# Performance work log

Measured on AMD Instinct MI355X. Metric: run time of the kernel, lower is better.

## Reference

```python
import jax, jax.numpy as jnp
import numpy as np

EMBED_DIM = 768
HEAD_SIZE = 64

def setup_inputs() -> dict:
    key = jax.random.key(0)
    k1, k2, k3, k4 = jax.random.split(key, 4)
    x = jax.random.normal(k1, (4, 4096, EMBED_DIM), dtype=jnp.float32)
    # nn.Linear(E, H, bias=False) weights, stored as [E, H] for y = x @ W
    scale = 1.0 / np.sqrt(EMBED_DIM)
    Wk = jax.random.uniform(k2, (EMBED_DIM, HEAD_SIZE), jnp.float32, -scale, scale)
    Wq = jax.random.uniform(k3, (EMBED_DIM, HEAD_SIZE), jnp.float32, -scale, scale)
    Wv = jax.random.uniform(k4, (EMBED_DIM, HEAD_SIZE), jnp.float32, -scale, scale)
    return {"x": x, "Wk": Wk, "Wq": Wq, "Wv": Wv}

def reference(x, Wk, Wq, Wv):
    # x: [B, S, E]
    E = x.shape[2]
    K = jnp.einsum("bse,eh->bsh", x, Wk)  # [B, S, H]
    Q = jnp.einsum("bse,eh->bsh", x, Wq)
    V = jnp.einsum("bse,eh->bsh", x, Wv)
    # NOTE: original scales by embedding_dim**0.5, not head_size**0.5
    A = jnp.einsum("bqh,bkh->bqk", Q, K) / jnp.sqrt(jnp.asarray(E, x.dtype))
    A = jax.nn.softmax(A, axis=-1)
    # dropout is inference-mode identity
    return jnp.einsum("bqk,bkh->bqh", A, V)
```

## Files before the change

### kernel.cpp

```cpp
#include <hip/hip_runtime.h>

typedef __attribute__((ext_vector_type(8))) short short8;
typedef __attribute__((ext_vector_type(4))) short short4v;
typedef __attribute__((ext_vector_type(4))) float float4v;

__device__ __forceinline__ short f2bf(float f) {
    union { float f; unsigned u; } v; v.f = f;
    return (short)((v.u + 0x7fffu + ((v.u >> 16) & 1u)) >> 16);
}

__device__ __forceinline__ float fast_exp2(float x) {
#if __has_builtin(__builtin_amdgcn_exp2f)
    return __builtin_amdgcn_exp2f(x);
#else
    return exp2f(x);
#endif
}

__global__ void wtrans_kernel(const float* __restrict__ Wk, const float* __restrict__ Wq,
                              const float* __restrict__ Wv, short* __restrict__ Wt3T) {
    int idx = blockIdx.x * 256 + threadIdx.x;
    int p = idx / 12288;
    int rem = idx - p * 12288;
    int kstep = rem / 512;
    int r2 = rem - kstep * 512;
    int lane = r2 >> 3, i = r2 & 7;
    int quad = lane >> 4, l16 = lane & 15;
    int j = p >> 2, nt = p & 3;
    int n = nt * 16 + l16;
    int k = kstep * 32 + quad * 8 + i;
    const float* W = (j == 0) ? Wq : (j == 1 ? Wk : Wv);
    float scale = (j == 0) ? 0.05205877f : 1.0f;
    Wt3T[idx] = f2bf(W[k * 64 + n] * scale);
}

__global__ __launch_bounds__(256, 4) void proj_kernel(
    const float* __restrict__ x, const short* __restrict__ Wt3T,
    short* __restrict__ Qs, short* __restrict__ Kb, short* __restrict__ Vtr)
{
    __shared__ alignas(16) int Abuf[3][256];
    __shared__ alignas(16) short sm[16 * 72];
    const int tid = threadIdx.x;
    const int wave = tid >> 6, lane = tid & 63, quad = lane >> 4, l16 = lane & 15;
    const int m0 = blockIdx.x * 16;
    const int p0 = wave * 3;

    const int xrow = tid >> 4, xcol = (tid & 15) * 2;
    const float* xp = x + (size_t)(m0 + xrow) * 768 + xcol;
    const int aidx = xrow * 16 + (tid & 15);
    const short* wt0 = Wt3T + (size_t)(p0 * 24) * 512 + lane * 8;

    float4v acc[3];
#pragma unroll
    for (int t = 0; t < 3; ++t) acc[t] = (float4v){0.f, 0.f, 0.f, 0.f};

    {
        float2 u = *(const float2*)xp;
        Abuf[0][aidx] = ((unsigned short)f2bf(u.x)) | ((unsigned)f2bf(u.y) << 16);
    }
    short8 Wc0 = *(const short8*)(wt0);
    short8 Wc1 = *(const short8*)(wt0 + 12288);
    short8 Wc2 = *(const short8*)(wt0 + 24576);
    float2 Xn = *(const float2*)(xp + 32);
    __syncthreads();

#pragma unroll
    for (int it = 0; it < 24; ++it) {
        short8 Wn0, Wn1, Wn2;
        float2 Xn2;
        if (it < 23) {
            const short* wn = wt0 + (it + 1) * 512;
            Wn0 = *(const short8*)(wn);
            Wn1 = *(const short8*)(wn + 12288);
            Wn2 = *(const short8*)(wn + 24576);
        }
        if (it < 22) Xn2 = *(const float2*)(xp + (it + 2) * 32);

        short8 a = *(const short8*)((const short*)Abuf[it % 3] + l16 * 32 + quad * 8);
        acc[0] = __builtin_amdgcn_mfma_f32_16x16x32_bf16(a, Wc0, acc[0], 0, 0, 0);
        acc[1] = __builtin_amdgcn_mfma_f32_16x16x32_bf16(a, Wc1, acc[1], 0, 0, 0);
        acc[2] = __builtin_amdgcn_mfma_f32_16x16x32_bf16(a, Wc2, acc[2], 0, 0, 0);

        if (it < 23)
            Abuf[(it + 1) % 3][aidx] = ((unsigned short)f2bf(Xn.x)) | ((unsigned)f2bf(Xn.y) << 16);
        Xn = Xn2;
        Wc0 = Wn0; Wc1 = Wn1; Wc2 = Wn2;
        __syncthreads();
    }

#pragma unroll
    for (int t = 0; t < 3; ++t) {
        const int p = p0 + t, j = p >> 2, nt = p & 3;
        if (j < 2) {
            short* dst = (j == 0) ? Qs : Kb;
#pragma unroll
            for (int r = 0; r < 4; ++r)
                dst[(size_t)(m0 + quad * 4 + r) * 64 + nt * 16 + l16] = f2bf(acc[t][r]);
        } else {
#pragma unroll
            for (int r = 0; r < 4; ++r)
                sm[(quad * 4 + r) * 72 + nt * 16 + l16] = f2bf(acc[t][r]);
        }
    }
    __syncthreads();
    {
        const int h = tid >> 2, si = (tid & 3) * 4;
        const int b = m0 >> 12, s0 = m0 & 4095;
        short4v tmp;
#pragma unroll
        for (int i = 0; i < 4; ++i) tmp[i] = sm[(si + i) * 72 + h];
        *(short4v*)(Vtr + (size_t)(b * 64 + h) * 4096 + s0 + si) = tmp;
    }
}

__global__ __launch_bounds__(256, 4) void attn_kernel(
    const short* __restrict__ Qs, const short* __restrict__ Kb, const short* __restrict__ Vt,
    float* __restrict__ Opart, float* __restrict__ Ll, int kv_len)
{
    __shared__ alignas(16) short Kl[64 * 72];
    __shared__ alignas(16) short Vl[64 * 72];
    __shared__ alignas(16) short Pl[4 * 32 * 72];

    const int tid = threadIdx.x;
    const int wave = tid >> 6, lane = tid & 63, quad = lane >> 4, l16 = lane & 15;
    const int qt = blockIdx.x, b = blockIdx.y, sp = blockIdx.z;
    const int q0 = qt * 128;
    const int bS = b * 4096;
    const int kv0 = sp * kv_len;

    short8 qa[2][2];
#pragma unroll
    for (int mt = 0; mt < 2; ++mt)
#pragma unroll
        for (int ks = 0; ks < 2; ++ks)
            qa[mt][ks] = *(const short8*)(Qs + (size_t)(bS + q0 + wave * 32 + mt * 16 + l16) * 64 + ks * 32 + quad * 8);

    float4v o[2][4];
    float rs[2][4];
#pragma unroll
    for (int mt = 0; mt < 2; ++mt)
#pragma unroll
        for (int nt = 0; nt < 4; ++nt) o[mt][nt] = (float4v){0.f, 0.f, 0.f, 0.f};
#pragma unroll
    for (int mt = 0; mt < 2; ++mt)
#pragma unroll
        for (int r = 0; r < 4; ++r) rs[mt][r] = 0.f;

    const int sr = tid >> 2, sc = (tid & 3) * 16;
    short* plw = &Pl[wave * 2304];

    for (int kt = 0; kt < kv_len; kt += 64) {
        const int kvg = kv0 + kt;
        __syncthreads();
        {
            const short* src = Kb + (size_t)(bS + kvg + sr) * 64 + sc;
            *(short8*)&Kl[sr * 72 + sc]     = *(const short8*)src;
            *(short8*)&Kl[sr * 72 + sc + 8] = *(const short8*)(src + 8);
            const short* vs = Vt + (size_t)(b * 64 + sr) * 4096 + kvg + sc;
            *(short8*)&Vl[sr * 72 + sc]     = *(const short8*)vs;
            *(short8*)&Vl[sr * 72 + sc + 8] = *(const short8*)(vs + 8);
        }
        __syncthreads();

        float4v s[2][4];
#pragma unroll
        for (int nt = 0; nt < 4; ++nt) {
            short8 b0 = *(const short8*)&Kl[(nt * 16 + l16) * 72 + quad * 8];
            short8 b1 = *(const short8*)&Kl[(nt * 16 + l16) * 72 + 32 + quad * 8];
#pragma unroll
            for (int mt = 0; mt < 2; ++mt) {
                float4v a0 = (float4v){0.f, 0.f, 0.f, 0.f};
                a0 = __builtin_amdgcn_mfma_f32_16x16x32_bf16(qa[mt][0], b0, a0, 0, 0, 0);
                a0 = __builtin_amdgcn_mfma_f32_16x16x32_bf16(qa[mt][1], b1, a0, 0, 0, 0);
                s[mt][nt] = a0;
            }
        }

#pragma unroll
        for (int mt = 0; mt < 2; ++mt)
#pragma unroll
            for (int nt = 0; nt < 4; ++nt)
#pragma unroll
                for (int r = 0; r < 4; ++r) {
                    float p = fast_exp2(s[mt][nt][r]);
                    rs[mt][r] += p;
                    plw[(mt * 16 + quad * 4 + r) * 72 + nt * 16 + l16] = f2bf(p);
                }

#pragma unroll
        for (int ks = 0; ks < 2; ++ks) {
            short8 bf[4];
#pragma unroll
            for (int nt = 0; nt < 4; ++nt)
                bf[nt] = *(const short8*)&Vl[(nt * 16 + l16) * 72 + ks * 32 + quad * 8];
#pragma unroll
            for (int mt = 0; mt < 2; ++mt) {
                short8 af = *(const short8*)&plw[(mt * 16 + l16) * 72 + ks * 32 + quad * 8];
#pragma unroll
                for (int nt = 0; nt < 4; ++nt)
                    o[mt][nt] = __builtin_amdgcn_mfma_f32_16x16x32_bf16(af, bf[nt], o[mt][nt], 0, 0, 0);
            }
        }
    }

#pragma unroll
    for (int mt = 0; mt < 2; ++mt)
#pragma unroll
        for (int r = 0; r < 4; ++r) {
#pragma unroll
            for (int off = 8; off >= 1; off >>= 1)
                rs[mt][r] += __shfl_xor(rs[mt][r], off);
        }

#pragma unroll
    for (int mt = 0; mt < 2; ++mt) {
#pragma unroll
        for (int nt = 0; nt < 4; ++nt)
#pragma unroll
            for (int r = 0; r < 4; ++r) {
                int qb = q0 + wave * 32 + mt * 16 + quad * 4 + r;
                Opart[((size_t)sp * 16384 + bS + qb) * 64 + nt * 16 + l16] = o[mt][nt][r];
            }
        if (l16 == 0) {
#pragma unroll
            for (int r = 0; r < 4; ++r) {
                int qb = q0 + wave * 32 + mt * 16 + quad * 4 + r;
                Ll[(size_t)sp * 16384 + bS + qb] = rs[mt][r];
            }
        }
    }
}

__global__ void combine_kernel(const float* __restrict__ Opart, const float* __restrict__ Ll,
                               float* __restrict__ out, int nsplit) {
    int idx = blockIdx.x * 256 + threadIdx.x;
    int q = idx >> 6;
    float den = 0.f, num = 0.f;
    for (int s = 0; s < nsplit; ++s) {
        den += Ll[s * 16384 + q];
        num += Opart[(size_t)s * 1048576 + idx];
    }
    out[idx] = num / den;
}

extern "C" void kernel_launch(void* const* d_in, const int* in_sizes, int n_in,
                              void* d_out, int out_size, void* d_ws, size_t ws_size,
                              hipStream_t stream) {
    const float* x  = (const float*)d_in[0];
    const float* Wk = (const float*)d_in[1];
    const float* Wq = (const float*)d_in[2];
    const float* Wv = (const float*)d_in[3];
    float* out = (float*)d_out;

    char* w = (char*)d_ws;
    size_t off = 0;
    auto take = [&](size_t bytes) -> void* {
        void* p = w + off;
        off = (off + bytes + 255) & ~(size_t)255;
        return p;
    };
    short* Qs  = (short*)take((size_t)16384 * 64 * 2);
    short* Kb  = (short*)take((size_t)16384 * 64 * 2);
    short* Vt  = (short*)take((size_t)16384 * 64 * 2);
    short* Wt3 = (short*)take((size_t)3 * 64 * 768 * 2);

    size_t base = off;
    int nsplit = 8;
    while (nsplit > 1) {
        size_t need = base + (((size_t)nsplit * 16384 * 4 + 255) & ~(size_t)255)
                      + (size_t)nsplit * 16384 * 64 * 4 + 512;
        if (need <= ws_size) break;
        nsplit >>= 1;
    }
    float* Ll    = (float*)take((size_t)nsplit * 16384 * 4);
    float* Opart = (float*)take((size_t)nsplit * 16384 * 64 * 4);

    wtrans_kernel<<<576, 256, 0, stream>>>(Wk, Wq, Wv, Wt3);
    proj_kernel<<<1024, 256, 0, stream>>>(x, Wt3, Qs, Kb, Vt);
    dim3 ag(32, 4, nsplit);
    attn_kernel<<<ag, 256, 0, stream>>>(Qs, Kb, Vt, Opart, Ll, 4096 / nsplit);
    combine_kernel<<<4096, 256, 0, stream>>>(Opart, Ll, out, nsplit);
}
```

Baseline: 144.8 us.

## Prefetch next K/V tile into registers and transpose S MFMA for packed P stores

Loads the next K and V tile from global memory into registers while the current tile is computed, replacing the load-then-wait pattern before each LDS fill. Swaps the MFMA operands so S is computed transposed: each lane then holds four consecutive keys for one query, which allows packed bf16 conversion with v_cvt_pk_bf16_f32 and 8-byte stores of P. The same layout shortens the row-sum reduction to two cross-lane shuffles. It also raises wave priority around the MFMA blocks. The prefetch adds register pressure under launch bounds of 4 blocks per CU.

```diff
diff --git a/kernel.cpp b/kernel.cpp
--- a/kernel.cpp
+++ b/kernel.cpp
@@ -3,6 +3,7 @@
 typedef __attribute__((ext_vector_type(8))) short short8;
 typedef __attribute__((ext_vector_type(4))) short short4v;
 typedef __attribute__((ext_vector_type(4))) float float4v;
+typedef __attribute__((ext_vector_type(2))) unsigned int uint2v;
 
 __device__ __forceinline__ short f2bf(float f) {
     union { float f; unsigned u; } v; v.f = f;
@@ -15,6 +16,12 @@
 #else
     return exp2f(x);
 #endif
+}
+
+__device__ __forceinline__ unsigned cvt_pk_bf16(float lo, float hi) {
+    unsigned r;
+    asm("v_cvt_pk_bf16_f32 %0, %1, %2" : "=v"(r) : "v"(lo), "v"(hi));
+    return r;
 }
 
 __global__ void wtrans_kernel(const float* __restrict__ Wk, const float* __restrict__ Wq,
@@ -128,64 +135,74 @@
     const int bS = b * 4096;
     const int kv0 = sp * kv_len;
 
-    short8 qa[2][2];
-#pragma unroll
-    for (int mt = 0; mt < 2; ++mt)
+    short8 qb[2][2];
+#pragma unroll
+    for (int ntq = 0; ntq < 2; ++ntq)
 #pragma unroll
         for (int ks = 0; ks < 2; ++ks)
-            qa[mt][ks] = *(const short8*)(Qs + (size_t)(bS + q0 + wave * 32 + mt * 16 + l16) * 64 + ks * 32 + quad * 8);
+            qb[ntq][ks] = *(const short8*)(Qs + (size_t)(bS + q0 + wave * 32 + ntq * 16 + l16) * 64 + ks * 32 + quad * 8);
 
     float4v o[2][4];
-    float rs[2][4];
-#pragma unroll
-    for (int mt = 0; mt < 2; ++mt)
-#pragma unroll
-        for (int nt = 0; nt < 4; ++nt) o[mt][nt] = (float4v){0.f, 0.f, 0.f, 0.f};
-#pragma unroll
-    for (int mt = 0; mt < 2; ++mt)
-#pragma unroll
-        for (int r = 0; r < 4; ++r) rs[mt][r] = 0.f;
+#pragma unroll
+    for (int ntq = 0; ntq < 2; ++ntq)
+#pragma unroll
+        for (int nt = 0; nt < 4; ++nt) o[ntq][nt] = (float4v){0.f, 0.f, 0.f, 0.f};
+    float rs[2] = {0.f, 0.f};
 
     const int sr = tid >> 2, sc = (tid & 3) * 16;
     short* plw = &Pl[wave * 2304];
 
-    for (int kt = 0; kt < kv_len; kt += 64) {
-        const int kvg = kv0 + kt;
+    const short* ksrc0 = Kb + (size_t)(bS + kv0 + sr) * 64 + sc;
+    const short* vsrc0 = Vt + (size_t)(b * 64 + sr) * 4096 + kv0 + sc;
+
+    short8 kr0 = *(const short8*)ksrc0;
+    short8 kr1 = *(const short8*)(ksrc0 + 8);
+    short8 vr0 = *(const short8*)vsrc0;
+    short8 vr1 = *(const short8*)(vsrc0 + 8);
+
+    const int ntiles = kv_len >> 6;
+    for (int t = 0; t < ntiles; ++t) {
         __syncthreads();
-        {
-            const short* src = Kb + (size_t)(bS + kvg + sr) * 64 + sc;
-            *(short8*)&Kl[sr * 72 + sc]     = *(const short8*)src;
-            *(short8*)&Kl[sr * 72 + sc + 8] = *(const short8*)(src + 8);
-            const short* vs = Vt + (size_t)(b * 64 + sr) * 4096 + kvg + sc;
-            *(short8*)&Vl[sr * 72 + sc]     = *(const short8*)vs;
-            *(short8*)&Vl[sr * 72 + sc + 8] = *(const short8*)(vs + 8);
-        }
+        *(short8*)&Kl[sr * 72 + sc]     = kr0;
+        *(short8*)&Kl[sr * 72 + sc + 8] = kr1;
+        *(short8*)&Vl[sr * 72 + sc]     = vr0;
+        *(short8*)&Vl[sr * 72 + sc + 8] = vr1;
         __syncthreads();
 
-        float4v s[2][4];
-#pragma unroll
-        for (int nt = 0; nt < 4; ++nt) {
-            short8 b0 = *(const short8*)&Kl[(nt * 16 + l16) * 72 + quad * 8];
-            short8 b1 = *(const short8*)&Kl[(nt * 16 + l16) * 72 + 32 + quad * 8];
-#pragma unroll
-            for (int mt = 0; mt < 2; ++mt) {
-                float4v a0 = (float4v){0.f, 0.f, 0.f, 0.f};
-                a0 = __builtin_amdgcn_mfma_f32_16x16x32_bf16(qa[mt][0], b0, a0, 0, 0, 0);
-                a0 = __builtin_amdgcn_mfma_f32_16x16x32_bf16(qa[mt][1], b1, a0, 0, 0, 0);
-                s[mt][nt] = a0;
-            }
-        }
-
-#pragma unroll
-        for (int mt = 0; mt < 2; ++mt)
-#pragma unroll
-            for (int nt = 0; nt < 4; ++nt)
-#pragma unroll
-                for (int r = 0; r < 4; ++r) {
-                    float p = fast_exp2(s[mt][nt][r]);
-                    rs[mt][r] += p;
-                    plw[(mt * 16 + quad * 4 + r) * 72 + nt * 16 + l16] = f2bf(p);
-                }
+        if (t + 1 < ntiles) {
+            const short* kn = ksrc0 + (size_t)(t + 1) * 4096;
+            kr0 = *(const short8*)kn;
+            kr1 = *(const short8*)(kn + 8);
+            const short* vn = vsrc0 + (t + 1) * 64;
+            vr0 = *(const short8*)vn;
+            vr1 = *(const short8*)(vn + 8);
+        }
+
+#pragma unroll
+        for (int mtk = 0; mtk < 4; ++mtk) {
+            short8 k0 = *(const short8*)&Kl[(mtk * 16 + l16) * 72 + quad * 8];
+            short8 k1 = *(const short8*)&Kl[(mtk * 16 + l16) * 72 + 32 + quad * 8];
+            float4v s0 = (float4v){0.f, 0.f, 0.f, 0.f};
+            float4v s1 = (float4v){0.f, 0.f, 0.f, 0.f};
+            __builtin_amdgcn_s_setprio(1);
+            s0 = __builtin_amdgcn_mfma_f32_16x16x32_bf16(k0, qb[0][0], s0, 0, 0, 0);
+            s0 = __builtin_amdgcn_mfma_f32_16x16x32_bf16(k1, qb[0][1], s0, 0, 0, 0);
+            s1 = __builtin_amdgcn_mfma_f32_16x16x32_bf16(k0, qb[1][0], s1, 0, 0, 0);
+            s1 = __builtin_amdgcn_mfma_f32_16x16x32_bf16(k1, qb[1][1], s1, 0, 0, 0);
+            __builtin_amdgcn_s_setprio(0);
+
+            float p00 = fast_exp2(s0[0]), p01 = fast_exp2(s0[1]);
+            float p02 = fast_exp2(s0[2]), p03 = fast_exp2(s0[3]);
+            float p10 = fast_exp2(s1[0]), p11 = fast_exp2(s1[1]);
+            float p12 = fast_exp2(s1[2]), p13 = fast_exp2(s1[3]);
+            rs[0] += (p00 + p01) + (p02 + p03);
+            rs[1] += (p10 + p11) + (p12 + p13);
+            uint2v w0, w1;
+            w0[0] = cvt_pk_bf16(p00, p01); w0[1] = cvt_pk_bf16(p02, p03);
+            w1[0] = cvt_pk_bf16(p10, p11); w1[1] = cvt_pk_bf16(p12, p13);
+            *(uint2v*)&plw[(l16) * 72 + mtk * 16 + quad * 4]      = w0;
+            *(uint2v*)&plw[(16 + l16) * 72 + mtk * 16 + quad * 4] = w1;
+        }
 
 #pragma unroll
         for (int ks = 0; ks < 2; ++ks) {
@@ -194,40 +211,34 @@
             for (int nt = 0; nt < 4; ++nt)
                 bf[nt] = *(const short8*)&Vl[(nt * 16 + l16) * 72 + ks * 32 + quad * 8];
 #pragma unroll
-            for (int mt = 0; mt < 2; ++mt) {
-                short8 af = *(const short8*)&plw[(mt * 16 + l16) * 72 + ks * 32 + quad * 8];
+            for (int ntq = 0; ntq < 2; ++ntq) {
+                short8 af = *(const short8*)&plw[(ntq * 16 + l16) * 72 + ks * 32 + quad * 8];
+                __builtin_amdgcn_s_setprio(1);
 #pragma unroll
                 for (int nt = 0; nt < 4; ++nt)
-                    o[mt][nt] = __builtin_amdgcn_mfma_f32_16x16x32_bf16(af, bf[nt], o[mt][nt], 0, 0, 0);
+                    o[ntq][nt] = __builtin_amdgcn_mfma_f32_16x16x32_bf16(af, bf[nt], o[ntq][nt], 0, 0, 0);
+                __builtin_amdgcn_s_setprio(0);
             }
         }
     }
 
 #pragma unroll
-    for (int mt = 0; mt < 2; ++mt)
-#pragma unroll
-        for (int r = 0; r < 4; ++r) {
-#pragma unroll
-            for (int off = 8; off >= 1; off >>= 1)
-                rs[mt][r] += __shfl_xor(rs[mt][r], off);
-        }
-
-#pragma unroll
-    for (int mt = 0; mt < 2; ++mt) {
+    for (int ntq = 0; ntq < 2; ++ntq) {
+        rs[ntq] += __shfl_xor(rs[ntq], 16);
+        rs[ntq] += __shfl_xor(rs[ntq], 32);
+    }
+
+#pragma unroll
+    for (int ntq = 0; ntq < 2; ++ntq) {
 #pragma unroll
         for (int nt = 0; nt < 4; ++nt)
 #pragma unroll
             for (int r = 0; r < 4; ++r) {
-                int qb = q0 + wave * 32 + mt * 16 + quad * 4 + r;
-                Opart[((size_t)sp * 16384 + bS + qb) * 64 + nt * 16 + l16] = o[mt][nt][r];
+                int qrow = q0 + wave * 32 + ntq * 16 + quad * 4 + r;
+                Opart[((size_t)sp * 16384 + bS + qrow) * 64 + nt * 16 + l16] = o[ntq][nt][r];
             }
-        if (l16 == 0) {
-#pragma unroll
-            for (int r = 0; r < 4; ++r) {
-                int qb = q0 + wave * 32 + mt * 16 + quad * 4 + r;
-                Ll[(size_t)sp * 16384 + bS + qb] = rs[mt][r];
-            }
-        }
+        if (quad == 0)
+            Ll[(size_t)sp * 16384 + bS + q0 + wave * 32 + ntq * 16 + l16] = rs[ntq];
     }
 }
 
```

Measured after the change: 138.2 us. -4.5%, faster.
